# Kernel tuning notes

Measured on AMD Instinct MI355X. Metric: run time of the kernel, lower is better.

## Reference

```python
import jax, jax.numpy as jnp
import numpy as np

N = 4096
INP_DIM = 256
EMB_DIM = 256
ALPHA = 0.01  # LeakyReLU negative slope
NEG_INF = -9.0e15


def _xavier(key, shape, gain=1.414):
    fan_in, fan_out = shape[0], shape[1]
    limit = gain * np.sqrt(6.0 / (fan_in + fan_out))
    return jax.random.uniform(key, shape, jnp.float32, -limit, limit)


def setup_inputs() -> dict:
    key = jax.random.key(0)
    ks = jax.random.split(key, 9)
    inp = {
        "input": jax.random.normal(ks[0], (N, INP_DIM), jnp.float32),
        "adj": jax.random.randint(ks[1], (N, N), 0, 2, jnp.int32),
        "W0": _xavier(ks[2], (INP_DIM, EMB_DIM)),
        "W1": _xavier(ks[3], (EMB_DIM, EMB_DIM)),
        "a1": _xavier(ks[4], (2 * EMB_DIM, 1)),
        "W2": _xavier(ks[5], (EMB_DIM, EMB_DIM)),
        "a2": _xavier(ks[6], (2 * EMB_DIM, 1)),
        "W3": _xavier(ks[7], (EMB_DIM, EMB_DIM)),
        "a3": _xavier(ks[8], (2 * EMB_DIM, 1)),
    }
    return inp


def _gat_layer(h, adj, W, a):
    # h: [N, F_in], W: [F_in, F], a: [2F, 1]
    Wh = h @ W                       # [N, F]
    F_out = Wh.shape[1]
    # e_ij = leakyrelu([Wh_i || Wh_j] @ a) = leakyrelu(Wh_i@a1 + Wh_j@a2)
    f1 = Wh @ a[:F_out]              # [N, 1]
    f2 = Wh @ a[F_out:]              # [N, 1]
    e = jax.nn.leaky_relu(f1 + f2.T, ALPHA)            # [N, N]
    att = jnp.where(adj > 0, e, NEG_INF)
    att = jax.nn.softmax(att, axis=1)                    # masked softmax over neighbors
    h_prime = att @ Wh                                   # [N, F]
    return jax.nn.elu(h_prime)                           # concat=True -> ELU


def reference(input, adj, W0, W1, a1, W2, a2, W3, a3):
    h = input @ W0                   # GAT-level projection
    h = _gat_layer(h, adj, W1, a1)
    h = _gat_layer(h, adj, W2, a2)
    h = _gat_layer(h, adj, W3, a3)
    return h
```

## Files before the change

### kernel.cpp

```cpp
#include <hip/hip_runtime.h>
#include <hip/hip_bf16.h>
#include <hip/hip_fp16.h>
#include <cstdint>
#include <cstddef>

#define NN 4096
#define WPR 64

typedef __attribute__((ext_vector_type(8))) unsigned short ushort8v;
typedef __attribute__((ext_vector_type(4))) unsigned short ushort4v;
typedef __attribute__((ext_vector_type(8))) short short8;
typedef __attribute__((ext_vector_type(4))) float float4v;

#define C1 30.0f
#define C2 0.3f

static __device__ __forceinline__ unsigned short f2bf(float x) {
    union { float f; unsigned int u; } v; v.f = x;
    unsigned int r = v.u + 0x7FFFu + ((v.u >> 16) & 1u);
    return (unsigned short)(r >> 16);
}

static __device__ __forceinline__ short8 as_s8(ushort8v v) {
    union { ushort8v u; short8 s; } x; x.u = v; return x.s;
}

static __device__ __forceinline__ void gl_lds16(const unsigned short* g, unsigned short* l) {
    __builtin_amdgcn_global_load_lds(
        (const __attribute__((address_space(1))) unsigned int*)g,
        (__attribute__((address_space(3))) unsigned int*)l,
        16, 0, 0);
}

__global__ __launch_bounds__(256) void setup_proj0(
    const float* __restrict__ input, const int* __restrict__ adj,
    const float* __restrict__ W0, const float* __restrict__ W2, const float* __restrict__ W3,
    unsigned long long* __restrict__ bits, unsigned short* __restrict__ h1,
    unsigned short* __restrict__ Wbt, float* __restrict__ f1f2)
{
    const int bid = blockIdx.x;
    const int t = threadIdx.x;
    const int lane = t & 63, wave = t >> 6;
    const int g = lane >> 4, ml = lane & 15;
    __shared__ unsigned short As[32 * 264];
    __shared__ unsigned short Bs[64 * 264];

    if (t < 48) f1f2[bid * 48 + t] = 0.f;
    {
        int idx = 131072 + bid * 256 + t;
        int within = idx & 65535;
        int n = within >> 8, k = within & 255;
        const float* W = ((idx >> 16) == 2) ? W2 : W3;
        Wbt[idx] = f2bf(W[k * 256 + n]);
    }
    const int m0 = (bid >> 2) * 32, n0 = (bid & 3) * 64;
    {
        int ar = t >> 3, ac0 = (t & 7) * 8;
        #pragma unroll
        for (int i = 0; i < 4; ++i) {
            int col = ac0 + i * 64;
            const float* src = &input[(size_t)(m0 + ar) * 256 + col];
            ushort8v v;
            #pragma unroll
            for (int j = 0; j < 8; ++j) v[j] = f2bf(src[j]);
            *(ushort8v*)&As[ar * 264 + col] = v;
        }
        #pragma unroll 8
        for (int it = 0; it < 64; ++it) {
            int k = it * 4 + wave;
            Bs[(t & 63) * 264 + k] = f2bf(W0[k * 256 + n0 + (t & 63)]);
        }
    }
    __syncthreads();
    {
        const int wm = (wave >> 1) * 16, wn = (wave & 1) * 32;
        float4v acc[2] = {{0.f,0.f,0.f,0.f},{0.f,0.f,0.f,0.f}};
        #pragma unroll
        for (int kk = 0; kk < 256; kk += 32) {
            const int kc = kk + g * 8;
            short8 a = as_s8(*(const ushort8v*)&As[(wm + ml) * 264 + kc]);
            #pragma unroll
            for (int fn = 0; fn < 2; ++fn) {
                short8 b = as_s8(*(const ushort8v*)&Bs[(wn + fn * 16 + ml) * 264 + kc]);
                acc[fn] = __builtin_amdgcn_mfma_f32_16x16x32_bf16(a, b, acc[fn], 0, 0, 0);
            }
        }
        const int rb = wm + g * 4;
        #pragma unroll
        for (int fn = 0; fn < 2; ++fn)
            #pragma unroll
            for (int r = 0; r < 4; ++r)
                h1[(size_t)(m0 + rb + r) * 256 + n0 + wn + fn * 16 + ml] = f2bf(acc[fn][r]);
    }
    {
        #pragma unroll 1
        for (int rr = 0; rr < 2; ++rr) {
            int row = bid * 8 + wave * 2 + rr;
            const int* arow = adj + (size_t)row * NN;
            #pragma unroll 8
            for (int seg = 0; seg < 64; ++seg) {
                unsigned long long m = __ballot(arow[seg * 64 + lane] > 0);
                if (lane == 0) bits[(size_t)row * WPR + seg] = m;
            }
        }
    }
}

__global__ __launch_bounds__(256) void proj1(
    const unsigned short* __restrict__ h1, const float* __restrict__ W1,
    const float* __restrict__ a1v, float* __restrict__ f1f2,
    unsigned short* __restrict__ Whbt)
{
    const int bid = blockIdx.x;
    const int t = threadIdx.x;
    const int lane = t & 63, wave = t >> 6;
    const int g = lane >> 4, ml = lane & 15;
    __shared__ unsigned short As[32 * 264];
    __shared__ unsigned short Bs[64 * 264];
    const int m0 = (bid >> 2) * 32, n0 = (bid & 3) * 64;
    {
        int ar = t >> 3, ac0 = (t & 7) * 8;
        #pragma unroll
        for (int i = 0; i < 4; ++i) {
            int col = ac0 + i * 64;
            *(ushort8v*)&As[ar * 264 + col] = *(const ushort8v*)&h1[(size_t)(m0 + ar) * 256 + col];
        }
        #pragma unroll 8
        for (int it = 0; it < 64; ++it) {
            int k = it * 4 + wave;
            Bs[(t & 63) * 264 + k] = f2bf(W1[k * 256 + n0 + (t & 63)]);
        }
    }
    __syncthreads();
    const int wm = (wave >> 1) * 16, wn = (wave & 1) * 32;
    float4v acc[2] = {{0.f,0.f,0.f,0.f},{0.f,0.f,0.f,0.f}};
    #pragma unroll
    for (int kk = 0; kk < 256; kk += 32) {
        const int kc = kk + g * 8;
        short8 a = as_s8(*(const ushort8v*)&As[(wm + ml) * 264 + kc]);
        #pragma unroll
        for (int fn = 0; fn < 2; ++fn) {
            short8 b = as_s8(*(const ushort8v*)&Bs[(wn + fn * 16 + ml) * 264 + kc]);
            acc[fn] = __builtin_amdgcn_mfma_f32_16x16x32_bf16(a, b, acc[fn], 0, 0, 0);
        }
    }
    const int rb = wm + g * 4;
    {
        float a1c[2], a2c[2];
        #pragma unroll
        for (int fn = 0; fn < 2; ++fn) {
            a1c[fn] = a1v[n0 + wn + fn * 16 + ml];
            a2c[fn] = a1v[256 + n0 + wn + fn * 16 + ml];
        }
        #pragma unroll
        for (int r = 0; r < 4; ++r) {
            float s1 = acc[0][r] * a1c[0] + acc[1][r] * a1c[1];
            float s2 = acc[0][r] * a2c[0] + acc[1][r] * a2c[1];
            #pragma unroll
            for (int off = 1; off < 16; off <<= 1) {
                s1 += __shfl_xor(s1, off, 64);
                s2 += __shfl_xor(s2, off, 64);
            }
            if (ml == 0) {
                int row = m0 + rb + r;
                atomicAdd(&f1f2[row], s1);
                atomicAdd(&f1f2[4096 + row], s2);
            }
        }
    }
    {
        unsigned short* T = As;
        __syncthreads();
        #pragma unroll
        for (int fn = 0; fn < 2; ++fn)
            #pragma unroll
            for (int r = 0; r < 4; ++r)
                T[(wn + fn * 16 + ml) * 40 + rb + r] = f2bf(acc[fn][r]);
        __syncthreads();
        const int tr = t >> 2, tc = (t & 3) * 8;
        *(ushort8v*)&Whbt[(size_t)(n0 + tr) * 4096 + m0 + tc] = *(const ushort8v*)&T[tr * 40 + tc];
    }
}

__global__ __launch_bounds__(256) void rowcoef(const unsigned long long* __restrict__ bits,
                                               const float* __restrict__ f1f2,
                                               float4* __restrict__ rowco,
                                               float2* __restrict__ tab2g) {
    __shared__ float2 tl[4096];
    const int t = threadIdx.x;
    const float* f2p = f1f2 + 4096;
    #pragma unroll
    for (int i = 0; i < 16; ++i) {
        float v = f2p[i * 256 + t];
        float2 pr = make_float2(__expf(v - C1), __expf(0.01f * v - C2));
        tl[i * 256 + t] = pr;
        if (blockIdx.x == 0) tab2g[i * 256 + t] = pr;
    }
    __syncthreads();
    const int lane = t & 63, wave = t >> 6;
    for (int rr = 0; rr < 2; ++rr) {
        const int row = blockIdx.x * 8 + wave * 2 + rr;
        const unsigned long long wl = bits[(size_t)row * WPR + lane];
        const float f1r = f1f2[row];
        const float th = __expf(-f1r - C1);
        float mx = 0.f, S1 = 0.f, S2 = 0.f;
        #pragma unroll 16
        for (int b = 0; b < 64; ++b) {
            unsigned long long w = __shfl(wl, b, 64);
            bool bit = (w >> lane) & 1ULL;
            float2 v = tl[b * 64 + lane];
            float ebm = bit ? v.x : 0.f;
            mx = fmaxf(mx, ebm);
            bool cond = v.x > th;
            S1 += (bit && cond)  ? v.x : 0.f;
            S2 += (bit && !cond) ? v.y : 0.f;
        }
        #pragma unroll
        for (int off = 1; off < 64; off <<= 1) {
            mx = fmaxf(mx, __shfl_xor(mx, off, 64));
            S1 += __shfl_xor(S1, off, 64);
            S2 += __shfl_xor(S2, off, 64);
        }
        if (lane == 0) {
            float M  = C1 + __logf(mx);
            float fm_ = f1r + M;
            float m  = fm_ > 0.f ? fm_ : 0.01f * fm_;
            float alpha = __expf(fminf(f1r + C1 - m, 60.f));
            float gamma = __expf(fminf(0.01f * (f1r + C1) - m, 60.f));
            float inv = 1.0f / (alpha * S1 + gamma * S2);
            rowco[row] = make_float4(alpha * inv, gamma * inv, th, 0.f);
        }
    }
}

template<int NSTEPS>
__global__ __launch_bounds__(256, 3) void att_gemm(const unsigned long long* __restrict__ bits,
                                                   const float4* __restrict__ rowco,
                                                   const float* __restrict__ tab2f,
                                                   const unsigned short* __restrict__ Bt,
                                                   unsigned short* __restrict__ parth) {
    const int t = threadIdx.x;
    const int bm = blockIdx.x & 31;
    const int bn = (blockIdx.x >> 5) & 1;
    const int ks = blockIdx.x >> 6;
    const int m0 = bm * 128, n0 = bn * 128;
    const int k0 = ks * (NSTEPS * 32);
    __shared__ unsigned short Bs[2][128 * 32];
    const int lane = t & 63, wave = t >> 6;
    const int g = lane >> 4, ml = lane & 15;

    const int drow = lane >> 2, dcol = ((lane & 3) ^ (lane >> 4)) * 8;
    const unsigned short* dsrc0 = Bt + (size_t)(n0 + wave * 16 + drow) * 4096 + dcol;
    const unsigned short* dsrc1 = dsrc0 + (size_t)64 * 4096;
    unsigned short* dst0 = &Bs[0][wave * 512];
    unsigned short* dst1 = &Bs[0][2048 + wave * 512];
    unsigned short* dst0b = &Bs[1][wave * 512];
    unsigned short* dst1b = &Bs[1][2048 + wave * 512];

    float pA[2], pG[2];
    unsigned long long wpre[2][NSTEPS / 2];
    #pragma unroll
    for (int fm = 0; fm < 2; ++fm) {
        int row = m0 + wave * 32 + fm * 16 + ml;
        float4 rc = rowco[row];
        pA[fm] = rc.x; pG[fm] = rc.y;
        const unsigned long long* brow = bits + (size_t)row * WPR + (k0 >> 6);
        #pragma unroll
        for (int w = 0; w < NSTEPS / 2; ++w) wpre[fm][w] = brow[w];
    }

    float4v acc[2][8];
    #pragma unroll
    for (int i = 0; i < 2; ++i)
        #pragma unroll
        for (int j = 0; j < 8; ++j) acc[i][j] = (float4v){0.f, 0.f, 0.f, 0.f};

    float4v tq0, tq1, tq2, tq3;
    {
        gl_lds16(dsrc0 + k0, dst0);
        gl_lds16(dsrc1 + k0, dst1);
        const float4v* q = (const float4v*)&tab2f[2 * (k0 + g * 8)];
        tq0 = q[0]; tq1 = q[1]; tq2 = q[2]; tq3 = q[3];
    }
    __syncthreads();

    const int rdoff = ((g ^ (ml >> 2)) & 3) * 8;

    #pragma unroll
    for (int i = 0; i < NSTEPS; ++i) {
        const int kk = k0 + i * 32;
        const int p = i & 1;
        float4v nt0, nt1, nt2, nt3;
        if (i + 1 < NSTEPS) {
            gl_lds16(dsrc0 + kk + 32, p ? dst0 : dst0b);
            gl_lds16(dsrc1 + kk + 32, p ? dst1 : dst1b);
            const float4v* q = (const float4v*)&tab2f[2 * (kk + 32 + g * 8)];
            nt0 = q[0]; nt1 = q[1]; nt2 = q[2]; nt3 = q[3];
        }
        const int sh = (i & 1) * 32 + g * 8;
        short8 afr[2];
        #pragma unroll
        for (int fm = 0; fm < 2; ++fm) {
            unsigned int wh = (unsigned int)(wpre[fm][i >> 1] >> sh);
            ushort8v af;
            #pragma unroll
            for (int jj = 0; jj < 4; ++jj) {
                float4v v = (jj == 0) ? tq0 : (jj == 1) ? tq1 : (jj == 2) ? tq2 : tq3;
                float x0 = fmaxf(pA[fm] * v[0], pG[fm] * v[1]);
                float x1 = fmaxf(pA[fm] * v[2], pG[fm] * v[3]);
                x0 = ((wh >> (2 * jj)) & 1u)     ? x0 : 0.f;
                x1 = ((wh >> (2 * jj + 1)) & 1u) ? x1 : 0.f;
                union { __hip_bfloat162 b2; unsigned int u; } cv;
                cv.b2 = __float22bfloat162_rn(make_float2(x0, x1));
                ((unsigned int*)&af)[jj] = cv.u;
            }
            afr[fm] = as_s8(af);
        }
        #pragma unroll
        for (int fn = 0; fn < 8; ++fn) {
            short8 b = as_s8(*(const ushort8v*)&Bs[p][(fn * 16 + ml) * 32 + rdoff]);
            acc[0][fn] = __builtin_amdgcn_mfma_f32_16x16x32_bf16(afr[0], b, acc[0][fn], 0, 0, 0);
            acc[1][fn] = __builtin_amdgcn_mfma_f32_16x16x32_bf16(afr[1], b, acc[1][fn], 0, 0, 0);
        }
        if (i + 1 < NSTEPS) {
            __syncthreads();
            tq0 = nt0; tq1 = nt1; tq2 = nt2; tq3 = nt3;
        }
    }

    unsigned short* pbase = parth + ((size_t)ks << 20) + (size_t)(bm * 2 + bn) * 16384;
    #pragma unroll
    for (int fm = 0; fm < 2; ++fm)
        #pragma unroll
        for (int fn = 0; fn < 8; ++fn) {
            ushort4v v4;
            #pragma unroll
            for (int r = 0; r < 4; ++r) {
                __half h = __float2half(acc[fm][fn][r]);
                v4[r] = *(unsigned short*)&h;
            }
            *(ushort4v*)&pbase[((wave * 16 + fm * 8 + fn) * 64 + lane) * 4] = v4;
        }
}

template<int NS>
__global__ __launch_bounds__(256) void fused_rp(const unsigned short* __restrict__ parth,
                                                const unsigned short* __restrict__ Bt,
                                                const float* __restrict__ av,
                                                float* __restrict__ f1f2,
                                                unsigned short* __restrict__ Cbt) {
    const int t = threadIdx.x;
    const int m0 = blockIdx.x * 16;
    __shared__ unsigned short hA[16 * 280];
    __shared__ unsigned short T[256 * 24];

    const int bmP = m0 >> 7;
    const int wavea = (m0 >> 5) & 3;
    const int fmP = (m0 >> 4) & 1;
    const int bn = t >> 7, fnc = (t >> 4) & 7;
    const int widx = wavea * 16 + fmP * 8 + fnc;
    const size_t cbase = (size_t)(bmP * 2 + bn) * 16384 + (size_t)widx * 256 + (t & 15) * 16;
    float s[16];
    #pragma unroll
    for (int e = 0; e < 16; ++e) s[e] = 0.f;
    #pragma unroll
    for (int sp = 0; sp < NS; ++sp) {
        const unsigned short* p = &parth[((size_t)sp << 20) + cbase];
        ushort8v v0 = *(const ushort8v*)p;
        ushort8v v1 = *(const ushort8v*)(p + 8);
        #pragma unroll
        for (int e = 0; e < 8; ++e) {
            unsigned short u0 = v0[e], u1 = v1[e];
            s[e]     += __half2float(*(__half*)&u0);
            s[8 + e] += __half2float(*(__half*)&u1);
        }
    }
    const int gq = (t & 15) >> 2;
    const int colb = bn * 128 + fnc * 16 + (t & 3) * 4;
    #pragma unroll
    for (int r = 0; r < 4; ++r) {
        ushort4v w4;
        #pragma unroll
        for (int c = 0; c < 4; ++c) {
            float x = s[c * 4 + r];
            x = x > 0.f ? x : (__expf(x) - 1.f);
            w4[c] = f2bf(x);
        }
        *(ushort4v*)&hA[(gq * 4 + r) * 280 + colb] = w4;
    }
    __syncthreads();

    const int lane = t & 63, wave = t >> 6;
    const int g = lane >> 4, ml = lane & 15;
    float4v acc[4] = {{0.f,0.f,0.f,0.f},{0.f,0.f,0.f,0.f},{0.f,0.f,0.f,0.f},{0.f,0.f,0.f,0.f}};
    #pragma unroll
    for (int kk = 0; kk < 256; kk += 32) {
        short8 a = as_s8(*(const ushort8v*)&hA[ml * 280 + kk + g * 8]);
        #pragma unroll
        for (int fn = 0; fn < 4; ++fn) {
            short8 b = as_s8(*(const ushort8v*)&Bt[(size_t)(wave * 64 + fn * 16 + ml) * 256 + kk + g * 8]);
            acc[fn] = __builtin_amdgcn_mfma_f32_16x16x32_bf16(a, b, acc[fn], 0, 0, 0);
        }
    }

    {
        float a1c[4], a2c[4];
        #pragma unroll
        for (int fn = 0; fn < 4; ++fn) {
            int col = wave * 64 + fn * 16 + ml;
            a1c[fn] = av[col];
            a2c[fn] = av[256 + col];
        }
        #pragma unroll
        for (int r = 0; r < 4; ++r) {
            float s1 = acc[0][r] * a1c[0] + acc[1][r] * a1c[1] + acc[2][r] * a1c[2] + acc[3][r] * a1c[3];
            float s2 = acc[0][r] * a2c[0] + acc[1][r] * a2c[1] + acc[2][r] * a2c[2] + acc[3][r] * a2c[3];
            #pragma unroll
            for (int off = 1; off < 16; off <<= 1) {
                s1 += __shfl_xor(s1, off, 64);
                s2 += __shfl_xor(s2, off, 64);
            }
            if (ml == 0) {
                int row = m0 + g * 4 + r;
                atomicAdd(&f1f2[row], s1);
                atomicAdd(&f1f2[4096 + row], s2);
            }
        }
    }

    #pragma unroll
    for (int fn = 0; fn < 4; ++fn) {
        int nl = wave * 64 + fn * 16 + ml;
        ushort4v v4;
        #pragma unroll
        for (int r = 0; r < 4; ++r) v4[r] = f2bf(acc[fn][r]);
        *(ushort4v*)&T[nl * 24 + g * 4] = v4;
    }
    __syncthreads();
    {
        const int tn = t >> 1, half = t & 1;
        #pragma unroll
        for (int pass = 0; pass < 2; ++pass) {
            int n = pass * 128 + tn;
            *(ushort8v*)&Cbt[(size_t)n * 4096 + m0 + half * 8] = *(const ushort8v*)&T[n * 24 + half * 8];
        }
    }
}

template<int NS>
__global__ __launch_bounds__(256) void reduce_out(const unsigned short* __restrict__ parth,
                                                  float* __restrict__ outf) {
    const int flat = (blockIdx.x * 256 + threadIdx.x) * 8;
    float s[8] = {0.f, 0.f, 0.f, 0.f, 0.f, 0.f, 0.f, 0.f};
    #pragma unroll
    for (int sp = 0; sp < NS; ++sp) {
        ushort8v v = *(const ushort8v*)&parth[((size_t)sp << 20) + flat];
        #pragma unroll
        for (int j = 0; j < 8; ++j) {
            unsigned short u = v[j];
            s[j] += __half2float(*(__half*)&u);
        }
    }
    const int tile  = flat >> 14;
    const int inner = flat & 16383;
    const int widx = inner >> 8;
    const int ls   = (inner >> 2) & 63;
    const int bm = tile >> 1, bn = tile & 1;
    const int wavea = widx >> 4, fm = (widx >> 3) & 1, fn = widx & 7;
    const int g = ls >> 4, ml = ls & 15;
    const int row0 = bm * 128 + wavea * 32 + fm * 16 + g * 4;
    const int col  = bn * 128 + fn * 16 + ml;
    #pragma unroll
    for (int r = 0; r < 4; ++r) {
        float x0 = s[r];
        float x1 = s[4 + r];
        x0 = x0 > 0.f ? x0 : (__expf(x0) - 1.f);
        x1 = x1 > 0.f ? x1 : (__expf(x1) - 1.f);
        *(float2*)&outf[(size_t)(row0 + r) * 256 + col] = make_float2(x0, x1);
    }
}

extern "C" void kernel_launch(void* const* d_in, const int* in_sizes, int n_in,
                              void* d_out, int out_size, void* d_ws, size_t ws_size,
                              hipStream_t stream) {
    const float* input = (const float*)d_in[0];
    const int*   adj   = (const int*)d_in[1];
    const float* W0    = (const float*)d_in[2];
    const float* W1    = (const float*)d_in[3];
    const float* a1    = (const float*)d_in[4];
    const float* W2    = (const float*)d_in[5];
    const float* a2    = (const float*)d_in[6];
    const float* W3    = (const float*)d_in[7];
    const float* a3    = (const float*)d_in[8];
    float* out = (float*)d_out;
    char* ws = (char*)d_ws;

    unsigned long long* bits = (unsigned long long*)(ws);
    unsigned short* h1   = (unsigned short*)(ws + (4u << 20));
    unsigned short* Whbt = (unsigned short*)(ws + (6u << 20));
    unsigned short* Wbt  = (unsigned short*)(ws + (8u << 20));
    float*  f1f2  = (float*)(ws + (9u << 20));
    float4* rowco = (float4*)(ws + (10u << 20));
    float2* tab2  = (float2*)(ws + (10u << 20) + (256u << 10));
    unsigned short* parth = (unsigned short*)(ws + (13u << 20));
    (void)ws_size;

    float* f1f2_l[3] = { f1f2, f1f2 + 8192, f1f2 + 16384 };

    setup_proj0<<<512, 256, 0, stream>>>(input, adj, W0, W2, W3, bits, h1, Wbt, f1f2);

    proj1<<<512, 256, 0, stream>>>(h1, W1, a1, f1f2_l[0], Whbt);
    rowcoef<<<512, 256, 0, stream>>>(bits, f1f2_l[0], rowco, tab2);
    att_gemm<16><<<512, 256, 0, stream>>>(bits, rowco, (const float*)tab2, Whbt, parth);

    fused_rp<8><<<256, 256, 0, stream>>>(parth, Wbt + 2 * 65536, a2, f1f2_l[1], Whbt);
    rowcoef<<<512, 256, 0, stream>>>(bits, f1f2_l[1], rowco, tab2);
    att_gemm<16><<<512, 256, 0, stream>>>(bits, rowco, (const float*)tab2, Whbt, parth);

    fused_rp<8><<<256, 256, 0, stream>>>(parth, Wbt + 3 * 65536, a3, f1f2_l[2], Whbt);
    rowcoef<<<512, 256, 0, stream>>>(bits, f1f2_l[2], rowco, tab2);
    att_gemm<16><<<512, 256, 0, stream>>>(bits, rowco, (const float*)tab2, Whbt, parth);
    reduce_out<8><<<512, 256, 0, stream>>>(parth, out);
}
```

Measured before the change: 311.1 us.

## Split setup kernel into role-specialized blocks and pretranspose W1 to bf16

The setup kernel now launches 5472 blocks, each doing one job: 4096 blocks pack one adjacency row each into bitmasks, then blocks for W1/W2/W3 bf16 transposition, zeroing f1f2, and the input@W0 projection. Before, each of 512 blocks did all of these jobs in sequence. Spreading the 64MB adj read over far more blocks is meant to raise memory-level parallelism. The layer-1 projection now reuses the generic proj_gemm with pre-transposed bf16 W1, so it no longer does strided fp32 loads of W1 in every block.

```diff
diff --git a/kernel.cpp b/kernel.cpp
--- a/kernel.cpp
+++ b/kernel.cpp
@@ -32,107 +32,110 @@
         16, 0, 0);
 }
 
-__global__ __launch_bounds__(256) void setup_proj0(
+__global__ __launch_bounds__(256) void setup_p0(
     const float* __restrict__ input, const int* __restrict__ adj,
-    const float* __restrict__ W0, const float* __restrict__ W2, const float* __restrict__ W3,
+    const float* __restrict__ W0, const float* __restrict__ W1,
+    const float* __restrict__ W2, const float* __restrict__ W3,
     unsigned long long* __restrict__ bits, unsigned short* __restrict__ h1,
     unsigned short* __restrict__ Wbt, float* __restrict__ f1f2)
 {
-    const int bid = blockIdx.x;
+    const int b = blockIdx.x;
     const int t = threadIdx.x;
-    const int lane = t & 63, wave = t >> 6;
-    const int g = lane >> 4, ml = lane & 15;
     __shared__ unsigned short As[32 * 264];
     __shared__ unsigned short Bs[64 * 264];
 
-    if (t < 48) f1f2[bid * 48 + t] = 0.f;
-    {
-        int idx = 131072 + bid * 256 + t;
+    if (b < 4096) {
+        const int wave = t >> 6, lane = t & 63;
+        const int* arow = adj + (size_t)b * NN;
+        #pragma unroll
+        for (int it = 0; it < NN / 256; ++it) {
+            int j = it * 256 + wave * 64 + lane;
+            unsigned long long m = __ballot(arow[j] > 0);
+            if (lane == 0) bits[(size_t)b * WPR + (it * 4 + wave)] = m;
+        }
+    } else if (b < 4864) {
+        int idx = (b - 4096) * 256 + t;
+        int mat = idx >> 16;
         int within = idx & 65535;
         int n = within >> 8, k = within & 255;
-        const float* W = ((idx >> 16) == 2) ? W2 : W3;
-        Wbt[idx] = f2bf(W[k * 256 + n]);
-    }
-    const int m0 = (bid >> 2) * 32, n0 = (bid & 3) * 64;
+        const float* W = (mat == 0) ? W1 : (mat == 1) ? W2 : W3;
+        Wbt[65536 + idx] = f2bf(W[k * 256 + n]);
+    } else if (b < 4960) {
+        f1f2[(b - 4864) * 256 + t] = 0.f;
+    } else {
+        const int bid2 = b - 4960;
+        const int lane = t & 63, wave = t >> 6;
+        const int g = lane >> 4, ml = lane & 15;
+        const int m0 = (bid2 >> 2) * 32, n0 = (bid2 & 3) * 64;
+        {
+            int ar = t >> 3, ac0 = (t & 7) * 8;
+            #pragma unroll
+            for (int i = 0; i < 4; ++i) {
+                int col = ac0 + i * 64;
+                const float* src = &input[(size_t)(m0 + ar) * 256 + col];
+                ushort8v v;
+                #pragma unroll
+                for (int j = 0; j < 8; ++j) v[j] = f2bf(src[j]);
+                *(ushort8v*)&As[ar * 264 + col] = v;
+            }
+            #pragma unroll 8
+            for (int it = 0; it < 64; ++it) {
+                int k = it * 4 + wave;
+                Bs[(t & 63) * 264 + k] = f2bf(W0[k * 256 + n0 + (t & 63)]);
+            }
+        }
+        __syncthreads();
+        {
+            const int wm = (wave >> 1) * 16, wn = (wave & 1) * 32;
+            float4v acc[2] = {{0.f,0.f,0.f,0.f},{0.f,0.f,0.f,0.f}};
+            #pragma unroll
+            for (int kk = 0; kk < 256; kk += 32) {
+                const int kc = kk + g * 8;
+                short8 a = as_s8(*(const ushort8v*)&As[(wm + ml) * 264 + kc]);
+                #pragma unroll
+                for (int fn = 0; fn < 2; ++fn) {
+                    short8 bfr = as_s8(*(const ushort8v*)&Bs[(wn + fn * 16 + ml) * 264 + kc]);
+                    acc[fn] = __builtin_amdgcn_mfma_f32_16x16x32_bf16(a, bfr, acc[fn], 0, 0, 0);
+                }
+            }
+            const int rb = wm + g * 4;
+            #pragma unroll
+            for (int fn = 0; fn < 2; ++fn)
+                #pragma unroll
+                for (int r = 0; r < 4; ++r)
+                    h1[(size_t)(m0 + rb + r) * 256 + n0 + wn + fn * 16 + ml] = f2bf(acc[fn][r]);
+        }
+    }
+}
+
+__global__ __launch_bounds__(256) void proj_gemm(const unsigned short* __restrict__ A,
+                                                 const unsigned short* __restrict__ Bt,
+                                                 const float* __restrict__ av,
+                                                 float* __restrict__ f1f2,
+                                                 unsigned short* __restrict__ Cbt) {
+    const int t = threadIdx.x;
+    const int bm = blockIdx.x >> 2, bn = blockIdx.x & 3;
+    const int m0 = bm * 32, n0 = bn * 64;
+    __shared__ unsigned short As[32 * 264];
+    __shared__ unsigned short Bs[64 * 264];
+    const int lane = t & 63, wave = t >> 6;
+    const int wm = (wave >> 1) * 16, wn = (wave & 1) * 32;
+    const int g = lane >> 4, ml = lane & 15;
     {
         int ar = t >> 3, ac0 = (t & 7) * 8;
         #pragma unroll
         for (int i = 0; i < 4; ++i) {
             int col = ac0 + i * 64;
-            const float* src = &input[(size_t)(m0 + ar) * 256 + col];
-            ushort8v v;
-            #pragma unroll
-            for (int j = 0; j < 8; ++j) v[j] = f2bf(src[j]);
-            *(ushort8v*)&As[ar * 264 + col] = v;
-        }
-        #pragma unroll 8
-        for (int it = 0; it < 64; ++it) {
-            int k = it * 4 + wave;
-            Bs[(t & 63) * 264 + k] = f2bf(W0[k * 256 + n0 + (t & 63)]);
+            *(ushort8v*)&As[ar * 264 + col] = *(const ushort8v*)&A[(size_t)(m0 + ar) * 256 + col];
+        }
+        int br = t >> 2, bc0 = (t & 3) * 8;
+        #pragma unroll
+        for (int i = 0; i < 8; ++i) {
+            int col = bc0 + i * 32;
+            *(ushort8v*)&Bs[br * 264 + col] = *(const ushort8v*)&Bt[(size_t)(n0 + br) * 256 + col];
         }
     }
     __syncthreads();
-    {
-        const int wm = (wave >> 1) * 16, wn = (wave & 1) * 32;
-        float4v acc[2] = {{0.f,0.f,0.f,0.f},{0.f,0.f,0.f,0.f}};
-        #pragma unroll
-        for (int kk = 0; kk < 256; kk += 32) {
-            const int kc = kk + g * 8;
-            short8 a = as_s8(*(const ushort8v*)&As[(wm + ml) * 264 + kc]);
-            #pragma unroll
-            for (int fn = 0; fn < 2; ++fn) {
-                short8 b = as_s8(*(const ushort8v*)&Bs[(wn + fn * 16 + ml) * 264 + kc]);
-                acc[fn] = __builtin_amdgcn_mfma_f32_16x16x32_bf16(a, b, acc[fn], 0, 0, 0);
-            }
-        }
-        const int rb = wm + g * 4;
-        #pragma unroll
-        for (int fn = 0; fn < 2; ++fn)
-            #pragma unroll
-            for (int r = 0; r < 4; ++r)
-                h1[(size_t)(m0 + rb + r) * 256 + n0 + wn + fn * 16 + ml] = f2bf(acc[fn][r]);
-    }
-    {
-        #pragma unroll 1
-        for (int rr = 0; rr < 2; ++rr) {
-            int row = bid * 8 + wave * 2 + rr;
-            const int* arow = adj + (size_t)row * NN;
-            #pragma unroll 8
-            for (int seg = 0; seg < 64; ++seg) {
-                unsigned long long m = __ballot(arow[seg * 64 + lane] > 0);
-                if (lane == 0) bits[(size_t)row * WPR + seg] = m;
-            }
-        }
-    }
-}
-
-__global__ __launch_bounds__(256) void proj1(
-    const unsigned short* __restrict__ h1, const float* __restrict__ W1,
-    const float* __restrict__ a1v, float* __restrict__ f1f2,
-    unsigned short* __restrict__ Whbt)
-{
-    const int bid = blockIdx.x;
-    const int t = threadIdx.x;
-    const int lane = t & 63, wave = t >> 6;
-    const int g = lane >> 4, ml = lane & 15;
-    __shared__ unsigned short As[32 * 264];
-    __shared__ unsigned short Bs[64 * 264];
-    const int m0 = (bid >> 2) * 32, n0 = (bid & 3) * 64;
-    {
-        int ar = t >> 3, ac0 = (t & 7) * 8;
-        #pragma unroll
-        for (int i = 0; i < 4; ++i) {
-            int col = ac0 + i * 64;
-            *(ushort8v*)&As[ar * 264 + col] = *(const ushort8v*)&h1[(size_t)(m0 + ar) * 256 + col];
-        }
-        #pragma unroll 8
-        for (int it = 0; it < 64; ++it) {
-            int k = it * 4 + wave;
-            Bs[(t & 63) * 264 + k] = f2bf(W1[k * 256 + n0 + (t & 63)]);
-        }
-    }
-    __syncthreads();
-    const int wm = (wave >> 1) * 16, wn = (wave & 1) * 32;
     float4v acc[2] = {{0.f,0.f,0.f,0.f},{0.f,0.f,0.f,0.f}};
     #pragma unroll
     for (int kk = 0; kk < 256; kk += 32) {
@@ -144,13 +147,14 @@
             acc[fn] = __builtin_amdgcn_mfma_f32_16x16x32_bf16(a, b, acc[fn], 0, 0, 0);
         }
     }
+
     const int rb = wm + g * 4;
     {
         float a1c[2], a2c[2];
         #pragma unroll
         for (int fn = 0; fn < 2; ++fn) {
-            a1c[fn] = a1v[n0 + wn + fn * 16 + ml];
-            a2c[fn] = a1v[256 + n0 + wn + fn * 16 + ml];
+            a1c[fn] = av[n0 + wn + fn * 16 + ml];
+            a2c[fn] = av[256 + n0 + wn + fn * 16 + ml];
         }
         #pragma unroll
         for (int r = 0; r < 4; ++r) {
@@ -168,6 +172,7 @@
             }
         }
     }
+
     {
         unsigned short* T = As;
         __syncthreads();
@@ -178,7 +183,7 @@
                 T[(wn + fn * 16 + ml) * 40 + rb + r] = f2bf(acc[fn][r]);
         __syncthreads();
         const int tr = t >> 2, tc = (t & 3) * 8;
-        *(ushort8v*)&Whbt[(size_t)(n0 + tr) * 4096 + m0 + tc] = *(const ushort8v*)&T[tr * 40 + tc];
+        *(ushort8v*)&Cbt[(size_t)(n0 + tr) * 4096 + m0 + tc] = *(const ushort8v*)&T[tr * 40 + tc];
     }
 }
 
@@ -507,9 +512,9 @@
 
     float* f1f2_l[3] = { f1f2, f1f2 + 8192, f1f2 + 16384 };
 
-    setup_proj0<<<512, 256, 0, stream>>>(input, adj, W0, W2, W3, bits, h1, Wbt, f1f2);
-
-    proj1<<<512, 256, 0, stream>>>(h1, W1, a1, f1f2_l[0], Whbt);
+    setup_p0<<<5472, 256, 0, stream>>>(input, adj, W0, W1, W2, W3, bits, h1, Wbt, f1f2);
+
+    proj_gemm<<<512, 256, 0, stream>>>(h1, Wbt + 1 * 65536, a1, f1f2_l[0], Whbt);
     rowcoef<<<512, 256, 0, stream>>>(bits, f1f2_l[0], rowco, tab2);
     att_gemm<16><<<512, 256, 0, stream>>>(bits, rowco, (const float*)tab2, Whbt, parth);
 
```

Measured after the change: 288.4 us. 1.08x faster.
